# Kernel tuning notes

Hardware: AMD Instinct MI355X
Metric: run time of the kernel (lower is better)

Reference implementation:

```python
import jax, jax.numpy as jnp
import numpy as np

EPS = 1e-5

def _ln(x, g, b):
    m = x.mean(-1, keepdims=True)
    v = jnp.var(x, axis=-1, keepdims=True)
    return (x - m) / jnp.sqrt(v + EPS) * g + b

def _forward(x, W_Q, W_K, W_V, W_O, ffn1_w, ffn1_b, ffn2_w, ffn2_b,
             ln1_g, ln1_b, ln2_g, ln2_b):
    B, C, H, W = x.shape
    nh, _, hd = W_Q.shape
    xl = x.transpose(0, 2, 3, 1)                      # [B,H,W,C]
    # per-head projections: [B,H,W,nh,hd]
    Q = jnp.einsum('bijc,hcd->bijhd', xl, W_Q)
    K = jnp.einsum('bijc,hcd->bijhd', xl, W_K)
    V = jnp.einsum('bijc,hcd->bijhd', xl, W_V)
    Hi, Wi = H - 2, W - 2
    Qc = Q[:, 1:H - 1, 1:W - 1]                       # interior queries
    # stack the 9 shifted views = 3x3 neighborhoods, row-major (i*3+j order)
    Kw = jnp.stack([K[:, di:di + Hi, dj:dj + Wi]
                    for di in range(3) for dj in range(3)], axis=3)  # [B,Hi,Wi,9,nh,hd]
    Vw = jnp.stack([V[:, di:di + Hi, dj:dj + Wi]
                    for di in range(3) for dj in range(3)], axis=3)
    scale = jnp.asarray(hd, x.dtype) ** 0.5
    attn = jnp.einsum('bijhd,bijnhd->bijnh', Qc, Kw) / scale
    attn = jax.nn.softmax(attn, axis=3)               # softmax over the 9 neighbors
    out = jnp.einsum('bijnh,bijnhd->bijhd', attn, Vw).reshape(B, Hi, Wi, nh * hd)
    out = out @ W_O                                   # output projection, [B,Hi,Wi,C]
    y = jnp.pad(out, ((0, 0), (1, 1), (1, 1), (0, 0)))  # border pixels stay zero
    y = jax.nn.relu(_ln(y, ln1_g, ln1_b))
    y = jax.nn.relu(y @ ffn1_w.T + ffn1_b)            # [B,H,W,9C]
    y = y @ ffn2_w.T + ffn2_b                         # [B,H,W,C]
    y = _ln(y, ln2_g, ln2_b)
    y = jax.nn.relu(y + xl)                           # identity shortcut (stride=1, C_in==C_out)
    return y.transpose(0, 3, 1, 2)                    # back to NCHW


def setup_inputs() -> dict:
    key = jax.random.key(0)
    ks = jax.random.split(key, 8)
    B, C, H, W, nh, hd = 8, 288, 48, 48, 9, 32
    Cff = C * 9
    f32 = jnp.float32
    return {
        'x': jax.random.normal(ks[0], (B, C, H, W), f32),
        'W_Q': jax.random.uniform(ks[1], (nh, C, hd), f32, -0.1, 0.1),
        'W_K': jax.random.uniform(ks[2], (nh, C, hd), f32, -0.1, 0.1),
        'W_V': jax.random.normal(ks[3], (nh, C, hd), f32) * 0.05,
        'W_O': jnp.eye(C, dtype=f32),
        'ffn1_w': jax.random.normal(ks[4], (Cff, C), f32) * 0.02,
        'ffn1_b': jnp.zeros((Cff,), f32),
        'ffn2_w': jax.random.normal(ks[5], (C, Cff), f32) * 0.02,
        'ffn2_b': jnp.zeros((C,), f32),
        'ln1_g': jnp.ones((C,), f32),
        'ln1_b': jnp.zeros((C,), f32),
        'ln2_g': jnp.ones((C,), f32),
        'ln2_b': jnp.zeros((C,), f32),
    }


def reference(x, W_Q, W_K, W_V, W_O, ffn1_w, ffn1_b, ffn2_w, ffn2_b,
              ln1_g, ln1_b, ln2_g, ln2_b):
    return _forward(x, W_Q, W_K, W_V, W_O, ffn1_w, ffn1_b, ffn2_w, ffn2_b,
                    ln1_g, ln1_b, ln2_g, ln2_b)
```

## Files before the change

### kernel.cpp

```cpp
#include <hip/hip_runtime.h>
#include <hip/hip_bf16.h>

static constexpr int Bn = 8, Cc = 288, Hh = 48, Ww = 48;
static constexpr int HW = Hh * Ww;
static constexpr int Mtot = Bn * HW;
static constexpr int NH = 9, HD = 32;
static constexpr int Cff = 2592;
static constexpr int CffP = 2688;
static constexpr int NQKV = 896;

typedef __attribute__((ext_vector_type(8))) short bf16x8;
typedef __attribute__((ext_vector_type(4))) float f32x4;
typedef __attribute__((ext_vector_type(4))) unsigned short u16x4;

typedef const __attribute__((address_space(1))) unsigned gmem_word;
typedef __attribute__((address_space(3))) unsigned lds_word;

__device__ __forceinline__ void gload16(const void* g, void* l) {
    __builtin_amdgcn_global_load_lds((gmem_word*)g, (lds_word*)l, 16, 0, 0);
}

template <int N>
__device__ __forceinline__ void vmwait() {
    asm volatile("s_waitcnt vmcnt(%0)" :: "n"(N) : "memory");
}

__device__ __forceinline__ int swz(int byte) {
    return byte ^ (((byte >> 7) & 7) << 4);
}

__device__ __forceinline__ float bf2f(unsigned short u) {
    return __bfloat162float(*(__hip_bfloat16*)&u);
}

__global__ __launch_bounds__(256) void transpose_in(const float* __restrict__ x,
                                                    __hip_bfloat16* __restrict__ xlb) {
    __shared__ float tile[32][33];
    int b = blockIdx.z;
    int c0 = blockIdx.y * 32;
    int p0 = blockIdx.x * 32;
    int tx = threadIdx.x, ty = threadIdx.y;
#pragma unroll
    for (int q = 0; q < 4; ++q) {
        int c = c0 + ty + q * 8;
        tile[ty + q * 8][tx] = x[((size_t)b * Cc + c) * HW + p0 + tx];
    }
    __syncthreads();
#pragma unroll
    for (int q = 0; q < 4; ++q) {
        int p = p0 + ty + q * 8;
        xlb[((size_t)b * HW + p) * Cc + c0 + tx] = __float2bfloat16(tile[tx][ty + q * 8]);
    }
}

__global__ __launch_bounds__(256) void prep_weights(const float* __restrict__ WQ,
                                                    const float* __restrict__ WK,
                                                    const float* __restrict__ WV,
                                                    const float* __restrict__ WO,
                                                    const float* __restrict__ f1w,
                                                    const float* __restrict__ f2w,
                                                    const float* __restrict__ f1b,
                                                    __hip_bfloat16* __restrict__ wqkvt,
                                                    __hip_bfloat16* __restrict__ wot,
                                                    __hip_bfloat16* __restrict__ w1b,
                                                    __hip_bfloat16* __restrict__ w2b,
                                                    float* __restrict__ b1p) {
    const int n1 = NQKV * Cc;
    const int n2 = n1 + Cc * Cc;
    const int n3 = n2 + CffP * Cc;
    const int n4 = n3 + Cc * CffP;
    const int n5 = n4 + CffP;
    int t = blockIdx.x * 256 + threadIdx.x;
    if (t < n1) {
        int n = t / Cc, c = t % Cc;
        float v = 0.f;
        if (n < 3 * Cc) {
            int g = n / Cc, r = n % Cc, h = r / HD, d = r % HD;
            const float* W = (g == 0) ? WQ : ((g == 1) ? WK : WV);
            v = W[((size_t)h * Cc + c) * HD + d];
        }
        wqkvt[t] = __float2bfloat16(v);
    } else if (t < n2) {
        int u = t - n1;
        int n = u / Cc, c = u % Cc;
        wot[u] = __float2bfloat16(WO[(size_t)c * Cc + n]);
    } else if (t < n3) {
        int u = t - n2;
        w1b[u] = __float2bfloat16(u < Cff * Cc ? f1w[u] : 0.f);
    } else if (t < n4) {
        int u = t - n3;
        int n = u / CffP, c = u % CffP;
        w2b[u] = __float2bfloat16(c < Cff ? f2w[(size_t)n * Cff + c] : 0.f);
    } else if (t < n5) {
        int u = t - n4;
        b1p[u] = (u < Cff) ? f1b[u] : 0.f;
    }
}

template <int BM, int BN, bool OUT_BF16, bool BIAS, bool RELU>
__global__ __launch_bounds__(256) void gemm_mfma(const __hip_bfloat16* __restrict__ A,
                                                 const __hip_bfloat16* __restrict__ Bw,
                                                 const float* __restrict__ bias,
                                                 void* __restrict__ Cout,
                                                 int M, int N, int K, int ldk) {
    constexpr int MR = BM / 32;
    constexpr int NF = BN / 32;
    constexpr int CA = BM / 16;
    constexpr int CB = BN / 16;
    constexpr int TOT = CA + CB;
    __shared__ __hip_bfloat16 As[2][BM * 32];
    __shared__ __hip_bfloat16 Bs[2][BN * 32];
    const int gx = gridDim.x, gy = gridDim.y;
    const int nwg = gx * gy * gridDim.z;
    int lin = blockIdx.x + gx * (blockIdx.y + gy * blockIdx.z);
    lin = (lin & 7) * (nwg >> 3) + (lin >> 3);
    const int bz = lin / (gx * gy);
    const int rem = lin - bz * gx * gy;
    const int by = rem / gx;
    const int bx = rem - by * gx;

    const int tid = threadIdx.x;
    const int wave = tid >> 6, lane = tid & 63;
    const int l16 = lane & 15, lq = lane >> 4;
    const int wr = wave >> 1, wc = wave & 1;
    const int bm = by * BM;
    const int bn = bx * BN;
    const int nt = K >> 5;
    const size_t kz2 = (size_t)bz * K * 2;
    const char* Ab = (const char*)A + kz2;
    const char* Bb = (const char*)Bw + kz2;
    const size_t ldk2 = (size_t)ldk * 2;

    f32x4 acc[MR][NF] = {};

    auto stage = [&](int buf, int t) {
        const size_t k0b = (size_t)(t << 5) * 2;
        for (int c = wave; c < TOT; c += 4) {
            if (c < CA) {
                int s = (c << 10) + lane * 16;
                int u = swz(s);
                int row = u >> 6, koff = u & 63;
                gload16(Ab + (size_t)(bm + row) * ldk2 + k0b + koff, &As[buf][c << 9]);
            } else {
                int s = ((c - CA) << 10) + lane * 16;
                int u = swz(s);
                int row = u >> 6, koff = u & 63;
                gload16(Bb + (size_t)(bn + row) * ldk2 + k0b + koff, &Bs[buf][(c - CA) << 9]);
            }
        }
    };

    int aoff[MR], boff[NF];
#pragma unroll
    for (int m = 0; m < MR; ++m)
        aoff[m] = swz((wr * (BM / 2) + m * 16 + l16) * 64 + lq * 16);
#pragma unroll
    for (int n = 0; n < NF; ++n)
        boff[n] = swz((wc * (BN / 2) + n * 16 + l16) * 64 + lq * 16);

    stage(0, 0);
    stage(1, 1);
    int cur = 0;
    for (int t = 0; t < nt; ++t) {
        if (t == nt - 1) {
            vmwait<0>();
        } else if constexpr ((TOT & 3) == 0) {
            vmwait<TOT / 4>();
        } else {
            if (wave < (TOT & 3)) vmwait<(TOT + 3) / 4>();
            else                  vmwait<TOT / 4>();
        }
        __builtin_amdgcn_s_barrier();
        const char* Ac = (const char*)&As[cur][0];
        const char* Bc = (const char*)&Bs[cur][0];
        bf16x8 a[MR], b[NF];
#pragma unroll
        for (int m = 0; m < MR; ++m) a[m] = *(const bf16x8*)(Ac + aoff[m]);
#pragma unroll
        for (int n = 0; n < NF; ++n) b[n] = *(const bf16x8*)(Bc + boff[n]);
        __builtin_amdgcn_s_setprio(1);
#pragma unroll
        for (int m = 0; m < MR; ++m)
#pragma unroll
            for (int n = 0; n < NF; ++n)
                acc[m][n] = __builtin_amdgcn_mfma_f32_16x16x32_bf16(a[m], b[n], acc[m][n], 0, 0, 0);
        __builtin_amdgcn_s_setprio(0);
        __builtin_amdgcn_s_barrier();
        if (t + 2 < nt) stage(cur, t + 2);
        cur ^= 1;
    }

    const size_t plane = (size_t)bz * M * N;
#pragma unroll
    for (int m = 0; m < MR; ++m) {
#pragma unroll
        for (int n = 0; n < NF; ++n) {
            const int col = bn + wc * (BN / 2) + n * 16 + l16;
            const float bv = BIAS ? bias[col] : 0.f;
#pragma unroll
            for (int r = 0; r < 4; ++r) {
                const int row = bm + wr * (BM / 2) + m * 16 + lq * 4 + r;
                float v = acc[m][n][r] + bv;
                if (RELU) v = fmaxf(v, 0.f);
                if (OUT_BF16)
                    ((__hip_bfloat16*)Cout)[plane + (size_t)row * N + col] = __float2bfloat16(v);
                else
                    ((float*)Cout)[plane + (size_t)row * N + col] = v;
            }
        }
    }
}

template <bool BIAS>
__global__ __launch_bounds__(256) void gemm_ln(const __hip_bfloat16* __restrict__ A,
                                               const __hip_bfloat16* __restrict__ Bw,
                                               const float* __restrict__ bias,
                                               const float* __restrict__ gam,
                                               const float* __restrict__ bet,
                                               __hip_bfloat16* __restrict__ dst,
                                               int K) {
    __shared__ __hip_bfloat16 As[2][32 * 32];
    __shared__ __hip_bfloat16 Bs[2][288 * 32];
    __shared__ float red[2][2][32];
    const int tid = threadIdx.x;
    const int wave = tid >> 6, lane = tid & 63;
    const int l16 = lane & 15, lq = lane >> 4;
    const int wr = wave >> 1, wc = wave & 1;
    const int bm = blockIdx.x * 32;
    const int nt = K >> 5;
    const char* Ab = (const char*)A;
    const char* Bb = (const char*)Bw;
    const size_t Ks2 = (size_t)K * 2;

    f32x4 acc[9] = {};

    auto stage = [&](int buf, int t) {
        const size_t k0b = (size_t)(t << 5) * 2;
        for (int c = wave; c < 20; c += 4) {
            if (c < 2) {
                int s = (c << 10) + lane * 16;
                int u = swz(s);
                int row = u >> 6, koff = u & 63;
                gload16(Ab + (size_t)(bm + row) * Ks2 + k0b + koff, &As[buf][c << 9]);
            } else {
                int s = ((c - 2) << 10) + lane * 16;
                int u = swz(s);
                int row = u >> 6, koff = u & 63;
                gload16(Bb + (size_t)row * Ks2 + k0b + koff, &Bs[buf][(c - 2) << 9]);
            }
        }
    };

    const int aoff = swz((wr * 16 + l16) * 64 + lq * 16);
    int boff[9];
#pragma unroll
    for (int n = 0; n < 9; ++n)
        boff[n] = swz((wc * 144 + n * 16 + l16) * 64 + lq * 16);

    stage(0, 0);
    stage(1, 1);
    int cur = 0;
    for (int t = 0; t < nt; ++t) {
        if (t == nt - 1) vmwait<0>();
        else             vmwait<5>();
        __builtin_amdgcn_s_barrier();
        const char* Ac = (const char*)&As[cur][0];
        const char* Bc = (const char*)&Bs[cur][0];
        bf16x8 a = *(const bf16x8*)(Ac + aoff);
        bf16x8 b[9];
#pragma unroll
        for (int n = 0; n < 9; ++n) b[n] = *(const bf16x8*)(Bc + boff[n]);
        __builtin_amdgcn_s_setprio(1);
#pragma unroll
        for (int n = 0; n < 9; ++n)
            acc[n] = __builtin_amdgcn_mfma_f32_16x16x32_bf16(a, b[n], acc[n], 0, 0, 0);
        __builtin_amdgcn_s_setprio(0);
        __builtin_amdgcn_s_barrier();
        if (t + 2 < nt) stage(cur, t + 2);
        cur ^= 1;
    }

    if (BIAS) {
#pragma unroll
        for (int n = 0; n < 9; ++n) {
            const float bv = bias[wc * 144 + n * 16 + l16];
#pragma unroll
            for (int r = 0; r < 4; ++r) acc[n][r] += bv;
        }
    }
    float sum[4] = {0.f, 0.f, 0.f, 0.f}, sq[4] = {0.f, 0.f, 0.f, 0.f};
#pragma unroll
    for (int n = 0; n < 9; ++n)
#pragma unroll
        for (int r = 0; r < 4; ++r) { sum[r] += acc[n][r]; sq[r] += acc[n][r] * acc[n][r]; }
#pragma unroll
    for (int s = 8; s >= 1; s >>= 1) {
#pragma unroll
        for (int r = 0; r < 4; ++r) { sum[r] += __shfl_xor(sum[r], s); sq[r] += __shfl_xor(sq[r], s); }
    }
    if (l16 == 0) {
#pragma unroll
        for (int r = 0; r < 4; ++r) {
            red[0][wc][wr * 16 + lq * 4 + r] = sum[r];
            red[1][wc][wr * 16 + lq * 4 + r] = sq[r];
        }
    }
    __syncthreads();
    float mean[4], rstd[4];
#pragma unroll
    for (int r = 0; r < 4; ++r) {
        const int rl = wr * 16 + lq * 4 + r;
        const float S = red[0][0][rl] + red[0][1][rl];
        const float Q = red[1][0][rl] + red[1][1][rl];
        mean[r] = S * (1.f / Cc);
        rstd[r] = rsqrtf(Q * (1.f / Cc) - mean[r] * mean[r] + 1e-5f);
    }
#pragma unroll
    for (int n = 0; n < 9; ++n) {
        const int col = wc * 144 + n * 16 + l16;
        const float gm = gam[col], bt = bet[col];
#pragma unroll
        for (int r = 0; r < 4; ++r) {
            const int row = bm + wr * 16 + lq * 4 + r;
            float y = (acc[n][r] - mean[r]) * rstd[r] * gm + bt;
            dst[(size_t)row * Cc + col] = __float2bfloat16(fmaxf(y, 0.f));
        }
    }
}

__global__ __launch_bounds__(256) void attn_kernel(const __hip_bfloat16* __restrict__ qkv,
                                                   __hip_bfloat16* __restrict__ aout) {
    int t = blockIdx.x * 256 + threadIdx.x;
    int d = t & 31;
    int ph = t >> 5;
    if (ph >= 16928 * 9) return;
    int h = ph % 9;
    int pix = ph / 9;
    int b = pix / (46 * 46);
    int r = pix % (46 * 46);
    int i = r / 46 + 1;
    int j = r % 46 + 1;
    int m = b * HW + i * Ww + j;
    int hd = h * HD + d;
    float q = __bfloat162float(qkv[(size_t)m * NQKV + hd]);
    float logits[9];
    int mns[9];
#pragma unroll
    for (int n = 0; n < 9; ++n) {
        int di = n / 3, dj = n % 3;
        int mn = b * HW + (i - 1 + di) * Ww + (j - 1 + dj);
        mns[n] = mn;
        float kv = __bfloat162float(qkv[(size_t)mn * NQKV + 288 + hd]);
        float p = q * kv;
#pragma unroll
        for (int s = 16; s >= 1; s >>= 1) p += __shfl_xor(p, s);
        logits[n] = p * 0.17677669529663687f;
    }
    float mx = logits[0];
#pragma unroll
    for (int n = 1; n < 9; ++n) mx = fmaxf(mx, logits[n]);
    float w[9];
    float sum = 0.f;
#pragma unroll
    for (int n = 0; n < 9; ++n) { w[n] = expf(logits[n] - mx); sum += w[n]; }
    float inv = 1.f / sum;
    float o = 0.f;
#pragma unroll
    for (int n = 0; n < 9; ++n)
        o += w[n] * __bfloat162float(qkv[(size_t)mns[n] * NQKV + 576 + hd]);
    aout[(size_t)m * Cc + hd] = __float2bfloat16(o * inv);
}

__global__ __launch_bounds__(256) void final_kernel(const __hip_bfloat16* __restrict__ part,
                                                    const float* __restrict__ fb2,
                                                    const __hip_bfloat16* __restrict__ xlb,
                                                    const float* __restrict__ g,
                                                    const float* __restrict__ bta,
                                                    float* __restrict__ out) {
    __shared__ float T[32][289];
    const int tid = threadIdx.x;
    const int wave = tid >> 6, lane = tid & 63;
    const int p0 = blockIdx.x * 32;
    const int b = p0 / HW;
    const int p = p0 % HW;
    const size_t plane = (size_t)Mtot * Cc;
    const unsigned short* pt = (const unsigned short*)part;
    const unsigned short* xr = (const unsigned short*)xlb;

    for (int it = 0; it < 8; ++it) {
        const int pw = wave * 8 + it;
        const size_t base = (size_t)(p0 + pw) * Cc;
        const int c0 = lane * 4;
        const int c1 = 256 + lane * 4;
        float v0[4], v1[4];
        {
            u16x4 a = *(const u16x4*)(pt + base + c0);
            u16x4 bb = *(const u16x4*)(pt + plane + base + c0);
            u16x4 cc = *(const u16x4*)(pt + 2 * plane + base + c0);
#pragma unroll
            for (int j = 0; j < 4; ++j)
                v0[j] = bf2f(a[j]) + bf2f(bb[j]) + bf2f(cc[j]) + fb2[c0 + j];
        }
        if (lane < 8) {
            u16x4 a = *(const u16x4*)(pt + base + c1);
            u16x4 bb = *(const u16x4*)(pt + plane + base + c1);
            u16x4 cc = *(const u16x4*)(pt + 2 * plane + base + c1);
#pragma unroll
            for (int j = 0; j < 4; ++j)
                v1[j] = bf2f(a[j]) + bf2f(bb[j]) + bf2f(cc[j]) + fb2[c1 + j];
        } else {
#pragma unroll
            for (int j = 0; j < 4; ++j) v1[j] = 0.f;
        }
        float sum = 0.f, sq = 0.f;
#pragma unroll
        for (int j = 0; j < 4; ++j) {
            sum += v0[j] + v1[j];
            sq += v0[j] * v0[j] + v1[j] * v1[j];
        }
#pragma unroll
        for (int s = 32; s >= 1; s >>= 1) { sum += __shfl_xor(sum, s); sq += __shfl_xor(sq, s); }
        const float mean = sum * (1.f / Cc);
        const float rstd = rsqrtf(sq * (1.f / Cc) - mean * mean + 1e-5f);
        {
            u16x4 xv = *(const u16x4*)(xr + base + c0);
#pragma unroll
            for (int j = 0; j < 4; ++j) {
                float y = (v0[j] - mean) * rstd * g[c0 + j] + bta[c0 + j];
                T[pw][c0 + j] = fmaxf(y + bf2f(xv[j]), 0.f);
            }
        }
        if (lane < 8) {
            u16x4 xv = *(const u16x4*)(xr + base + c1);
#pragma unroll
            for (int j = 0; j < 4; ++j) {
                float y = (v1[j] - mean) * rstd * g[c1 + j] + bta[c1 + j];
                T[pw][c1 + j] = fmaxf(y + bf2f(xv[j]), 0.f);
            }
        }
    }
    __syncthreads();
#pragma unroll
    for (int k = 0; k < 36; ++k) {
        const int idx = k * 256 + tid;
        const int c = idx >> 5, pw = idx & 31;
        out[((size_t)b * Cc + c) * HW + p + pw] = T[pw][c];
    }
}

__global__ void sentinel_kernel(float* out, float val) {
    out[threadIdx.x] = val;
}

extern "C" void kernel_launch(void* const* d_in, const int* in_sizes, int n_in,
                              void* d_out, int out_size, void* d_ws, size_t ws_size,
                              hipStream_t stream) {
    const float* x   = (const float*)d_in[0];
    const float* WQ  = (const float*)d_in[1];
    const float* WK  = (const float*)d_in[2];
    const float* WV  = (const float*)d_in[3];
    const float* WO  = (const float*)d_in[4];
    const float* f1w = (const float*)d_in[5];
    const float* f1b = (const float*)d_in[6];
    const float* f2w = (const float*)d_in[7];
    const float* f2b = (const float*)d_in[8];
    const float* g1  = (const float*)d_in[9];
    const float* b1  = (const float*)d_in[10];
    const float* g2  = (const float*)d_in[11];
    const float* b2  = (const float*)d_in[12];

    char* ws = (char*)d_ws;
    size_t off = 0;
    auto alloc = [&](size_t bytes) { void* p = ws + off; off += (bytes + 255) & ~(size_t)255; return p; };

    __hip_bfloat16* xlb   = (__hip_bfloat16*)alloc((size_t)Mtot * Cc * 2);
    __hip_bfloat16* wqkvt = (__hip_bfloat16*)alloc((size_t)NQKV * Cc * 2);
    __hip_bfloat16* qkv   = (__hip_bfloat16*)alloc((size_t)Mtot * NQKV * 2);
    __hip_bfloat16* aout  = (__hip_bfloat16*)alloc((size_t)Mtot * Cc * 2);
    __hip_bfloat16* wot   = (__hip_bfloat16*)alloc((size_t)Cc * Cc * 2);
    __hip_bfloat16* yln   = (__hip_bfloat16*)alloc((size_t)Mtot * Cc * 2);
    __hip_bfloat16* w1b   = (__hip_bfloat16*)alloc((size_t)CffP * Cc * 2);
    float*          b1p   = (float*)alloc((size_t)CffP * 4);
    __hip_bfloat16* mid   = (__hip_bfloat16*)alloc((size_t)Mtot * CffP * 2);
    __hip_bfloat16* w2b   = (__hip_bfloat16*)alloc((size_t)Cc * CffP * 2);
    __hip_bfloat16* f2o3  = (__hip_bfloat16*)alloc((size_t)3 * Mtot * Cc * 2);

    if (ws_size < off) {
        sentinel_kernel<<<1, 256, 0, stream>>>((float*)d_out, (float)off * 1e-6f);
        return;
    }

    transpose_in<<<dim3(HW / 32, Cc / 32, Bn), dim3(32, 8), 0, stream>>>(x, xlb);

    {
        const int total = NQKV * Cc + Cc * Cc + CffP * Cc + Cc * CffP + CffP;
        prep_weights<<<(total + 255) / 256, 256, 0, stream>>>(
            WQ, WK, WV, WO, f1w, f2w, f1b, wqkvt, wot, w1b, w2b, b1p);
    }

    gemm_mfma<96, 128, true, false, false><<<dim3(NQKV / 128, Mtot / 96, 1), 256, 0, stream>>>(
        xlb, wqkvt, nullptr, qkv, Mtot, NQKV, Cc, Cc);

    hipMemsetAsync(aout, 0, (size_t)Mtot * Cc * 2, stream);
    attn_kernel<<<(16928 * 9 * 32) / 256, 256, 0, stream>>>(qkv, aout);

    gemm_ln<false><<<Mtot / 32, 256, 0, stream>>>(
        aout, wot, nullptr, g1, b1, yln, Cc);

    gemm_mfma<128, 128, true, true, true><<<dim3(CffP / 128, Mtot / 128, 1), 256, 0, stream>>>(
        yln, w1b, b1p, mid, Mtot, CffP, Cc, Cc);

    gemm_mfma<96, 96, true, false, false><<<dim3(Cc / 96, Mtot / 96, 3), 256, 0, stream>>>(
        mid, w2b, nullptr, f2o3, Mtot, Cc, CffP / 3, CffP);

    final_kernel<<<Mtot / 32, 256, 0, stream>>>(f2o3, f2b, xlb, g2, b2, (float*)d_out);
}
```

Baseline: 210.2 us.

## Drop padding in QKV and FFN buffers and vectorize attention loads

Removes the column padding of the QKV projection (896 to 864) and of the FFN hidden dimension (2688 to 2592) in the stored intermediates. The QKV GEMM switches to 96x96 tiles and the FFN2 GEMM reduces over the unpadded K. The GEMM epilogue gains a store-column bound and a leading-dimension argument so FFN1 can still compute padded tiles while writing only real columns. The attention kernel now has each thread handle 4 head dims with 8-byte vector loads and a 3-step shuffle reduction, cutting thread count and the 5-step shuffle, at the cost of smaller, less aligned rows and a K split of 864 that must still fit the tile schedule.

```diff
diff --git a/kernel.cpp b/kernel.cpp
--- a/kernel.cpp
+++ b/kernel.cpp
@@ -7,7 +7,7 @@
 static constexpr int NH = 9, HD = 32;
 static constexpr int Cff = 2592;
 static constexpr int CffP = 2688;
-static constexpr int NQKV = 896;
+static constexpr int NQ = 864;
 
 typedef __attribute__((ext_vector_type(8))) short bf16x8;
 typedef __attribute__((ext_vector_type(4))) float f32x4;
@@ -31,6 +31,11 @@
 
 __device__ __forceinline__ float bf2f(unsigned short u) {
     return __bfloat162float(*(__hip_bfloat16*)&u);
+}
+
+__device__ __forceinline__ unsigned short f2bf(float f) {
+    __hip_bfloat16 h = __float2bfloat16(f);
+    return *(unsigned short*)&h;
 }
 
 __global__ __launch_bounds__(256) void transpose_in(const float* __restrict__ x,
@@ -65,21 +70,17 @@
                                                     __hip_bfloat16* __restrict__ w1b,
                                                     __hip_bfloat16* __restrict__ w2b,
                                                     float* __restrict__ b1p) {
-    const int n1 = NQKV * Cc;
+    const int n1 = NQ * Cc;
     const int n2 = n1 + Cc * Cc;
     const int n3 = n2 + CffP * Cc;
-    const int n4 = n3 + Cc * CffP;
+    const int n4 = n3 + Cc * Cff;
     const int n5 = n4 + CffP;
     int t = blockIdx.x * 256 + threadIdx.x;
     if (t < n1) {
         int n = t / Cc, c = t % Cc;
-        float v = 0.f;
-        if (n < 3 * Cc) {
-            int g = n / Cc, r = n % Cc, h = r / HD, d = r % HD;
-            const float* W = (g == 0) ? WQ : ((g == 1) ? WK : WV);
-            v = W[((size_t)h * Cc + c) * HD + d];
-        }
-        wqkvt[t] = __float2bfloat16(v);
+        int g = n / Cc, r = n % Cc, h = r / HD, d = r % HD;
+        const float* W = (g == 0) ? WQ : ((g == 1) ? WK : WV);
+        wqkvt[t] = __float2bfloat16(W[((size_t)h * Cc + c) * HD + d]);
     } else if (t < n2) {
         int u = t - n1;
         int n = u / Cc, c = u % Cc;
@@ -89,8 +90,7 @@
         w1b[u] = __float2bfloat16(u < Cff * Cc ? f1w[u] : 0.f);
     } else if (t < n4) {
         int u = t - n3;
-        int n = u / CffP, c = u % CffP;
-        w2b[u] = __float2bfloat16(c < Cff ? f2w[(size_t)n * Cff + c] : 0.f);
+        w2b[u] = __float2bfloat16(f2w[u]);
     } else if (t < n5) {
         int u = t - n4;
         b1p[u] = (u < Cff) ? f1b[u] : 0.f;
@@ -102,7 +102,8 @@
                                                  const __hip_bfloat16* __restrict__ Bw,
                                                  const float* __restrict__ bias,
                                                  void* __restrict__ Cout,
-                                                 int M, int N, int K, int ldk) {
+                                                 int M, int N, int K, int ldk,
+                                                 int nstore, int ldc) {
     constexpr int MR = BM / 32;
     constexpr int NF = BN / 32;
     constexpr int CA = BM / 16;
@@ -190,22 +191,24 @@
         cur ^= 1;
     }
 
-    const size_t plane = (size_t)bz * M * N;
+    const size_t plane = (size_t)bz * M * ldc;
 #pragma unroll
     for (int m = 0; m < MR; ++m) {
 #pragma unroll
         for (int n = 0; n < NF; ++n) {
             const int col = bn + wc * (BN / 2) + n * 16 + l16;
-            const float bv = BIAS ? bias[col] : 0.f;
-#pragma unroll
-            for (int r = 0; r < 4; ++r) {
-                const int row = bm + wr * (BM / 2) + m * 16 + lq * 4 + r;
-                float v = acc[m][n][r] + bv;
-                if (RELU) v = fmaxf(v, 0.f);
-                if (OUT_BF16)
-                    ((__hip_bfloat16*)Cout)[plane + (size_t)row * N + col] = __float2bfloat16(v);
-                else
-                    ((float*)Cout)[plane + (size_t)row * N + col] = v;
+            if (col < nstore) {
+                const float bv = BIAS ? bias[col] : 0.f;
+#pragma unroll
+                for (int r = 0; r < 4; ++r) {
+                    const int row = bm + wr * (BM / 2) + m * 16 + lq * 4 + r;
+                    float v = acc[m][n][r] + bv;
+                    if (RELU) v = fmaxf(v, 0.f);
+                    if (OUT_BF16)
+                        ((__hip_bfloat16*)Cout)[plane + (size_t)row * ldc + col] = __float2bfloat16(v);
+                    else
+                        ((float*)Cout)[plane + (size_t)row * ldc + col] = v;
+                }
             }
         }
     }
@@ -331,8 +334,8 @@
 __global__ __launch_bounds__(256) void attn_kernel(const __hip_bfloat16* __restrict__ qkv,
                                                    __hip_bfloat16* __restrict__ aout) {
     int t = blockIdx.x * 256 + threadIdx.x;
-    int d = t & 31;
-    int ph = t >> 5;
+    int l8 = t & 7;
+    int ph = t >> 3;
     if (ph >= 16928 * 9) return;
     int h = ph % 9;
     int pix = ph / 9;
@@ -341,8 +344,10 @@
     int i = r / 46 + 1;
     int j = r % 46 + 1;
     int m = b * HW + i * Ww + j;
-    int hd = h * HD + d;
-    float q = __bfloat162float(qkv[(size_t)m * NQKV + hd]);
+    int hd = h * HD + l8 * 4;
+    const unsigned short* qp = (const unsigned short*)qkv;
+    u16x4 qv = *(const u16x4*)(qp + (size_t)m * NQ + hd);
+    float q0 = bf2f(qv[0]), q1 = bf2f(qv[1]), q2 = bf2f(qv[2]), q3 = bf2f(qv[3]);
     float logits[9];
     int mns[9];
 #pragma unroll
@@ -350,10 +355,11 @@
         int di = n / 3, dj = n % 3;
         int mn = b * HW + (i - 1 + di) * Ww + (j - 1 + dj);
         mns[n] = mn;
-        float kv = __bfloat162float(qkv[(size_t)mn * NQKV + 288 + hd]);
-        float p = q * kv;
-#pragma unroll
-        for (int s = 16; s >= 1; s >>= 1) p += __shfl_xor(p, s);
+        u16x4 kv = *(const u16x4*)(qp + (size_t)mn * NQ + 288 + hd);
+        float p = q0 * bf2f(kv[0]) + q1 * bf2f(kv[1]) + q2 * bf2f(kv[2]) + q3 * bf2f(kv[3]);
+        p += __shfl_xor(p, 1);
+        p += __shfl_xor(p, 2);
+        p += __shfl_xor(p, 4);
         logits[n] = p * 0.17677669529663687f;
     }
     float mx = logits[0];
@@ -364,11 +370,19 @@
 #pragma unroll
     for (int n = 0; n < 9; ++n) { w[n] = expf(logits[n] - mx); sum += w[n]; }
     float inv = 1.f / sum;
-    float o = 0.f;
-#pragma unroll
-    for (int n = 0; n < 9; ++n)
-        o += w[n] * __bfloat162float(qkv[(size_t)mns[n] * NQKV + 576 + hd]);
-    aout[(size_t)m * Cc + hd] = __float2bfloat16(o * inv);
+    float o0 = 0.f, o1 = 0.f, o2 = 0.f, o3 = 0.f;
+#pragma unroll
+    for (int n = 0; n < 9; ++n) {
+        u16x4 vv = *(const u16x4*)(qp + (size_t)mns[n] * NQ + 576 + hd);
+        o0 += w[n] * bf2f(vv[0]);
+        o1 += w[n] * bf2f(vv[1]);
+        o2 += w[n] * bf2f(vv[2]);
+        o3 += w[n] * bf2f(vv[3]);
+    }
+    u16x4 ov;
+    ov[0] = f2bf(o0 * inv); ov[1] = f2bf(o1 * inv);
+    ov[2] = f2bf(o2 * inv); ov[3] = f2bf(o3 * inv);
+    *(u16x4*)((unsigned short*)aout + (size_t)m * Cc + hd) = ov;
 }
 
 __global__ __launch_bounds__(256) void final_kernel(const __hip_bfloat16* __restrict__ part,
@@ -474,15 +488,15 @@
     auto alloc = [&](size_t bytes) { void* p = ws + off; off += (bytes + 255) & ~(size_t)255; return p; };
 
     __hip_bfloat16* xlb   = (__hip_bfloat16*)alloc((size_t)Mtot * Cc * 2);
-    __hip_bfloat16* wqkvt = (__hip_bfloat16*)alloc((size_t)NQKV * Cc * 2);
-    __hip_bfloat16* qkv   = (__hip_bfloat16*)alloc((size_t)Mtot * NQKV * 2);
+    __hip_bfloat16* wqkvt = (__hip_bfloat16*)alloc((size_t)NQ * Cc * 2);
+    __hip_bfloat16* qkv   = (__hip_bfloat16*)alloc((size_t)Mtot * NQ * 2);
     __hip_bfloat16* aout  = (__hip_bfloat16*)alloc((size_t)Mtot * Cc * 2);
     __hip_bfloat16* wot   = (__hip_bfloat16*)alloc((size_t)Cc * Cc * 2);
     __hip_bfloat16* yln   = (__hip_bfloat16*)alloc((size_t)Mtot * Cc * 2);
     __hip_bfloat16* w1b   = (__hip_bfloat16*)alloc((size_t)CffP * Cc * 2);
     float*          b1p   = (float*)alloc((size_t)CffP * 4);
-    __hip_bfloat16* mid   = (__hip_bfloat16*)alloc((size_t)Mtot * CffP * 2);
-    __hip_bfloat16* w2b   = (__hip_bfloat16*)alloc((size_t)Cc * CffP * 2);
+    __hip_bfloat16* mid   = (__hip_bfloat16*)alloc((size_t)Mtot * Cff * 2);
+    __hip_bfloat16* w2b   = (__hip_bfloat16*)alloc((size_t)Cc * Cff * 2);
     __hip_bfloat16* f2o3  = (__hip_bfloat16*)alloc((size_t)3 * Mtot * Cc * 2);
 
     if (ws_size < off) {
@@ -493,25 +507,25 @@
     transpose_in<<<dim3(HW / 32, Cc / 32, Bn), dim3(32, 8), 0, stream>>>(x, xlb);
 
     {
-        const int total = NQKV * Cc + Cc * Cc + CffP * Cc + Cc * CffP + CffP;
+        const int total = NQ * Cc + Cc * Cc + CffP * Cc + Cc * Cff + CffP;
         prep_weights<<<(total + 255) / 256, 256, 0, stream>>>(
             WQ, WK, WV, WO, f1w, f2w, f1b, wqkvt, wot, w1b, w2b, b1p);
     }
 
-    gemm_mfma<96, 128, true, false, false><<<dim3(NQKV / 128, Mtot / 96, 1), 256, 0, stream>>>(
-        xlb, wqkvt, nullptr, qkv, Mtot, NQKV, Cc, Cc);
+    gemm_mfma<96, 96, true, false, false><<<dim3(NQ / 96, Mtot / 96, 1), 256, 0, stream>>>(
+        xlb, wqkvt, nullptr, qkv, Mtot, NQ, Cc, Cc, NQ, NQ);
 
     hipMemsetAsync(aout, 0, (size_t)Mtot * Cc * 2, stream);
-    attn_kernel<<<(16928 * 9 * 32) / 256, 256, 0, stream>>>(qkv, aout);
+    attn_kernel<<<(16928 * 9 * 8) / 256, 256, 0, stream>>>(qkv, aout);
 
     gemm_ln<false><<<Mtot / 32, 256, 0, stream>>>(
         aout, wot, nullptr, g1, b1, yln, Cc);
 
     gemm_mfma<128, 128, true, true, true><<<dim3(CffP / 128, Mtot / 128, 1), 256, 0, stream>>>(
-        yln, w1b, b1p, mid, Mtot, CffP, Cc, Cc);
+        yln, w1b, b1p, mid, Mtot, CffP, Cc, Cc, Cff, Cff);
 
     gemm_mfma<96, 96, true, false, false><<<dim3(Cc / 96, Mtot / 96, 3), 256, 0, stream>>>(
-        mid, w2b, nullptr, f2o3, Mtot, Cc, CffP / 3, CffP);
+        mid, w2b, nullptr, f2o3, Mtot, Cc, Cff / 3, Cff, Cc, Cc);
 
     final_kernel<<<Mtot / 32, 256, 0, stream>>>(f2o3, f2b, xlb, g2, b2, (float*)d_out);
 }
```

After: 201.2 us. 4.3% less time.
